# Kernel tuning notes

Hardware: AMD Instinct MI355X
Metric: run time of the kernel (lower is better)

The kernel has to match this reference:

```python
import jax, jax.numpy as jnp
import numpy as np

FEATURE_DIM = 256
NUM_STEPS = 3
NUM_GRAPHS = 2048
ATOMS_PER_GRAPH = 64
TOTAL_ATOMS = NUM_GRAPHS * ATOMS_PER_GRAPH


def setup_inputs() -> dict:
    key = jax.random.key(0)
    k_x, k1, k2, k3, k4 = jax.random.split(key, 5)
    H = FEATURE_DIM
    s = 1.0 / np.sqrt(H)
    x = jax.random.normal(k_x, (TOTAL_ATOMS, H), dtype=jnp.float32)
    batch = jnp.repeat(jnp.arange(NUM_GRAPHS, dtype=jnp.int64), ATOMS_PER_GRAPH)
    sizes = jnp.full((NUM_GRAPHS,), ATOMS_PER_GRAPH, dtype=jnp.int64)
    # LSTM params (PyTorch layout: gates ordered i, f, g, o)
    W_ih = jax.random.uniform(k1, (4 * H, H), jnp.float32, -s, s)
    W_hh = jax.random.uniform(k2, (4 * H, H), jnp.float32, -s, s)
    b_ih = jax.random.uniform(k3, (4 * H,), jnp.float32, -s, s)
    b_hh = jax.random.uniform(k4, (4 * H,), jnp.float32, -s, s)
    return {"x": x, "batch": batch, "sizes": sizes,
            "W_ih": W_ih, "W_hh": W_hh, "b_ih": b_ih, "b_hh": b_hh}


def _lstm_cell(u, hx, cx, W_ih, W_hh, b_ih, b_hh):
    # u: input [B,H]; (hx, cx): hidden/cell [B,H]
    gates = u @ W_ih.T + b_ih + hx @ W_hh.T + b_hh  # [B, 4H]
    i, f, g, o = jnp.split(gates, 4, axis=-1)
    i, f, o = jax.nn.sigmoid(i), jax.nn.sigmoid(f), jax.nn.sigmoid(o)
    c = f * cx + i * jnp.tanh(g)
    h = o * jnp.tanh(c)
    return h, c


def _segment_softmax(scores, seg, num_segments):
    m = jax.ops.segment_max(scores, seg, num_segments=num_segments)
    e = jnp.exp(scores - m[seg])
    s = jax.ops.segment_sum(e, seg, num_segments=num_segments)
    return e / s[seg]


def reference(x, batch, sizes, W_ih, W_hh, b_ih, b_hh):
    B = sizes.shape[0]
    H = x.shape[1]
    seg = batch.astype(jnp.int32)
    h = jnp.zeros((B, H), dtype=x.dtype)
    c = jnp.zeros((B, H), dtype=x.dtype)
    q = h
    r = h
    for _ in range(NUM_STEPS):
        # torch code feeds h both as LSTM input and hidden state
        q, c = _lstm_cell(h, h, c, W_ih, W_hh, b_ih, b_hh)
        scores = jnp.sum(x * q[seg], axis=-1)              # [total_atoms]
        attn = _segment_softmax(scores, seg, B)            # per-graph softmax
        r = jax.ops.segment_sum(x * attn[:, None], seg, num_segments=B)  # [B,H]
        h = r  # torch code overwrites the LSTM hidden with r
    return jnp.concatenate([q, r], axis=-1)  # [B, 2H]
```

## Files before the change

kernel.cpp:

```cpp
#include <hip/hip_runtime.h>
#include <math.h>

#define H 256
#define NB 2048
#define APG 64

typedef __attribute__((ext_vector_type(8))) short short8;
typedef __attribute__((ext_vector_type(4))) float f32x4;

__device__ __forceinline__ unsigned short f2bf(float f) {
    unsigned u = __float_as_uint(f);
    u += 0x7fff + ((u >> 16) & 1);
    return (unsigned short)(u >> 16);
}
__device__ __forceinline__ float bf2f(unsigned short s) {
    return __uint_as_float((unsigned)s << 16);
}
__device__ __forceinline__ float sigm(float v) { return 1.f / (1.f + __expf(-v)); }

__global__ void prep_kernel(const float* __restrict__ W_ih, const float* __restrict__ W_hh,
                            const float* __restrict__ b_ih, const float* __restrict__ b_hh,
                            unsigned short* __restrict__ Wr, float* __restrict__ br) {
    int idx = blockIdx.x * 256 + threadIdx.x;
    int wr_row = idx >> 8, k = idx & 255;
    int hcol = wr_row >> 2, gate = wr_row & 3;
    int src = gate * 65536 + hcol * 256 + k;
    Wr[idx] = f2bf(W_ih[src] + W_hh[src]);
    if (idx < 1024) {
        int hc = idx >> 2, gt = idx & 3;
        br[idx] = b_ih[gt * 256 + hc] + b_hh[gt * 256 + hc];
    }
}

__global__ void lstm0(const float* __restrict__ br, float* __restrict__ q1,
                      float* __restrict__ c1) {
    int hc = threadIdx.x;
    float gi = br[hc * 4 + 0], gg = br[hc * 4 + 2], go = br[hc * 4 + 3];
    float si = sigm(gi), so = sigm(go);
    float cn = si * tanhf(gg);
    c1[hc] = cn;
    q1[hc] = so * tanhf(cn);
}

__global__ __launch_bounds__(256)
void gemm_lstm(const unsigned short* __restrict__ hbf, const unsigned short* __restrict__ Wr,
               const float* __restrict__ br, float* __restrict__ c,
               float* __restrict__ qdst, int qstride) {
    __shared__ unsigned short smem[2][64 * 128];
    unsigned short* As = smem[0];
    unsigned short* Bs = smem[1];
    int t = threadIdx.x;
    int r0 = blockIdx.y * 64;
    int w0 = blockIdx.x * 64;
    int c0h = blockIdx.x * 16;
    int lane = t & 63, w = t >> 6;
    int ln = lane & 15, qd = lane >> 4;
    int m0 = w * 16;
    f32x4 acc[4] = {};
    for (int kc = 0; kc < 2; ++kc) {
        #pragma unroll
        for (int p = 0; p < 4; ++p) {
            int gid = p * 256 + t;
            int row = gid >> 4, g = gid & 15;
            int sg = g ^ (row & 15);
            *(short8*)&As[row * 128 + sg * 8] =
                *(const short8*)&hbf[(r0 + row) * H + kc * 128 + g * 8];
            *(short8*)&Bs[row * 128 + sg * 8] =
                *(const short8*)&Wr[(w0 + row) * H + kc * 128 + g * 8];
        }
        __syncthreads();
        #pragma unroll
        for (int kk = 0; kk < 4; ++kk) {
            int ga = (kk * 4 + qd) ^ ln;
            short8 a = *(short8*)&As[(m0 + ln) * 128 + ga * 8];
            #pragma unroll
            for (int t4 = 0; t4 < 4; ++t4) {
                short8 b = *(short8*)&Bs[(t4 * 16 + ln) * 128 + ga * 8];
                acc[t4] = __builtin_amdgcn_mfma_f32_16x16x32_bf16(a, b, acc[t4], 0, 0, 0);
            }
        }
        __syncthreads();
    }
    float* gl = (float*)smem;
    #pragma unroll
    for (int t4 = 0; t4 < 4; ++t4)
        #pragma unroll
        for (int r = 0; r < 4; ++r)
            gl[(m0 + qd * 4 + r) * 68 + t4 * 16 + ln] = acc[t4][r];
    __syncthreads();
    #pragma unroll
    for (int p = 0; p < 4; ++p) {
        int idx = p * 256 + t;
        int row = idx >> 4, hc = idx & 15;
        float4 g4 = *(float4*)&gl[row * 68 + hc * 4];
        float4 b4 = *(const float4*)&br[(c0h + hc) * 4];
        float gi = g4.x + b4.x, gf = g4.y + b4.y, gg = g4.z + b4.z, go = g4.w + b4.w;
        float si = sigm(gi), sf = sigm(gf), so = sigm(go);
        int cidx = (r0 + row) * H + c0h + hc;
        float cn = sf * c[cidx] + si * tanhf(gg);
        c[cidx] = cn;
        qdst[(r0 + row) * qstride + c0h + hc] = so * tanhf(cn);
    }
}

__global__ __launch_bounds__(256)
void attention1(const float* __restrict__ x, const float* __restrict__ q1,
                unsigned short* __restrict__ hbf, const float* __restrict__ c1,
                float* __restrict__ cdst, unsigned short* __restrict__ xbf) {
    __shared__ float sc[64];
    __shared__ float pl[64];
    __shared__ float rpart[4][256];
    int g = blockIdx.x, t = threadIdx.x;
    int lane = t & 63, w = t >> 6;
    const float* xg = x + (size_t)g * APG * H;
    unsigned short* xbg = xbf + (size_t)g * APG * H;
    float4 xa[16];
    #pragma unroll
    for (int i = 0; i < 16; ++i)
        xa[i] = *(const float4*)&xg[(i * 4 + w) * H + lane * 4];
    float4 q4 = *(const float4*)&q1[lane * 4];
    cdst[g * H + t] = c1[t];
    #pragma unroll
    for (int i = 0; i < 16; ++i) {
        ushort4 u;
        u.x = f2bf(xa[i].x); u.y = f2bf(xa[i].y);
        u.z = f2bf(xa[i].z); u.w = f2bf(xa[i].w);
        *(ushort4*)&xbg[(i * 4 + w) * H + lane * 4] = u;
    }
    #pragma unroll
    for (int i = 0; i < 16; ++i) {
        float p = xa[i].x * q4.x + xa[i].y * q4.y + xa[i].z * q4.z + xa[i].w * q4.w;
        #pragma unroll
        for (int s = 32; s > 0; s >>= 1) p += __shfl_xor(p, s, 64);
        if (lane == 0) sc[i * 4 + w] = p;
    }
    __syncthreads();
    if (t < 64) {
        float s = sc[t], m = s;
        #pragma unroll
        for (int d = 32; d > 0; d >>= 1) m = fmaxf(m, __shfl_xor(m, d, 64));
        float e = __expf(s - m), sum = e;
        #pragma unroll
        for (int d = 32; d > 0; d >>= 1) sum += __shfl_xor(sum, d, 64);
        pl[t] = e / sum;
    }
    __syncthreads();
    float4 r4 = {0.f, 0.f, 0.f, 0.f};
    #pragma unroll
    for (int i = 0; i < 16; ++i) {
        float p = pl[i * 4 + w];
        r4.x += p * xa[i].x; r4.y += p * xa[i].y;
        r4.z += p * xa[i].z; r4.w += p * xa[i].w;
    }
    *(float4*)&rpart[w][lane * 4] = r4;
    __syncthreads();
    float o = rpart[0][t] + rpart[1][t] + rpart[2][t] + rpart[3][t];
    hbf[g * H + t] = f2bf(o);
}

__global__ __launch_bounds__(256)
void attention_bf(const unsigned short* __restrict__ xbf, const float* __restrict__ qsrc,
                  int qstride, unsigned short* __restrict__ hbf,
                  float* __restrict__ rf32, int rstride) {
    __shared__ float sc[64];
    __shared__ float pl[64];
    __shared__ float rpart[4][256];
    int g = blockIdx.x, t = threadIdx.x;
    int lane = t & 63, w = t >> 6;
    const unsigned short* xg = xbf + (size_t)g * APG * H;
    ushort4 xa[16];
    #pragma unroll
    for (int i = 0; i < 16; ++i)
        xa[i] = *(const ushort4*)&xg[(i * 4 + w) * H + lane * 4];
    float4 q4 = *(const float4*)&qsrc[g * qstride + lane * 4];
    #pragma unroll
    for (int i = 0; i < 16; ++i) {
        float p = bf2f(xa[i].x) * q4.x + bf2f(xa[i].y) * q4.y
                + bf2f(xa[i].z) * q4.z + bf2f(xa[i].w) * q4.w;
        #pragma unroll
        for (int s = 32; s > 0; s >>= 1) p += __shfl_xor(p, s, 64);
        if (lane == 0) sc[i * 4 + w] = p;
    }
    __syncthreads();
    if (t < 64) {
        float s = sc[t], m = s;
        #pragma unroll
        for (int d = 32; d > 0; d >>= 1) m = fmaxf(m, __shfl_xor(m, d, 64));
        float e = __expf(s - m), sum = e;
        #pragma unroll
        for (int d = 32; d > 0; d >>= 1) sum += __shfl_xor(sum, d, 64);
        pl[t] = e / sum;
    }
    __syncthreads();
    float4 r4 = {0.f, 0.f, 0.f, 0.f};
    #pragma unroll
    for (int i = 0; i < 16; ++i) {
        float p = pl[i * 4 + w];
        r4.x += p * bf2f(xa[i].x); r4.y += p * bf2f(xa[i].y);
        r4.z += p * bf2f(xa[i].z); r4.w += p * bf2f(xa[i].w);
    }
    *(float4*)&rpart[w][lane * 4] = r4;
    __syncthreads();
    float o = rpart[0][t] + rpart[1][t] + rpart[2][t] + rpart[3][t];
    if (hbf)  hbf[g * H + t] = f2bf(o);
    if (rf32) rf32[g * rstride + t] = o;
}

extern "C" void kernel_launch(void* const* d_in, const int* in_sizes, int n_in,
                              void* d_out, int out_size, void* d_ws, size_t ws_size,
                              hipStream_t stream) {
    const float* x    = (const float*)d_in[0];
    const float* W_ih = (const float*)d_in[3];
    const float* W_hh = (const float*)d_in[4];
    const float* b_ih = (const float*)d_in[5];
    const float* b_hh = (const float*)d_in[6];
    float* out = (float*)d_out;

    char* ws = (char*)d_ws;
    unsigned short* Wr   = (unsigned short*)ws;
    float*          br   = (float*)(ws + 524288);
    unsigned short* hbf  = (unsigned short*)(ws + 528384);
    float*          cbuf = (float*)(ws + 1576960);
    float*          qbuf = (float*)(ws + 3674112);
    float*          q1   = (float*)(ws + 5771264);
    float*          c1   = (float*)(ws + 5772288);
    unsigned short* xbf  = (unsigned short*)(ws + 8388608);

    prep_kernel<<<1024, 256, 0, stream>>>(W_ih, W_hh, b_ih, b_hh, Wr, br);
    lstm0<<<1, 256, 0, stream>>>(br, q1, c1);
    attention1<<<2048, 256, 0, stream>>>(x, q1, hbf, c1, cbuf, xbf);
    gemm_lstm<<<dim3(16, 32), 256, 0, stream>>>(hbf, Wr, br, cbuf, qbuf, 256);
    attention_bf<<<2048, 256, 0, stream>>>(xbf, qbuf, 256, hbf, nullptr, 0);
    gemm_lstm<<<dim3(16, 32), 256, 0, stream>>>(hbf, Wr, br, cbuf, out, 512);
    attention_bf<<<2048, 256, 0, stream>>>(xbf, out, 512, nullptr, out + 256, 512);
}
```

Before: 267.1 us.

## Stream fp32 x in every attention pass instead of caching a bf16 copy

Drops the global bf16 copy of x, which was written once and read twice. Each attention pass now reads fp32 x directly, stages a bf16 copy in shared memory for the weighted sum, and computes scores in fp32. Initial cell-state broadcast moves into a separate 2048-block lstm0b kernel. This removes the 64MB bf16 write but raises each later pass's x read from 64MB to 128MB, and the 32KB shared-memory tile may reduce occupancy.

```diff
diff --git a/kernel.cpp b/kernel.cpp
--- a/kernel.cpp
+++ b/kernel.cpp
@@ -32,14 +32,14 @@
     }
 }
 
-__global__ void lstm0(const float* __restrict__ br, float* __restrict__ q1,
-                      float* __restrict__ c1) {
-    int hc = threadIdx.x;
-    float gi = br[hc * 4 + 0], gg = br[hc * 4 + 2], go = br[hc * 4 + 3];
-    float si = sigm(gi), so = sigm(go);
-    float cn = si * tanhf(gg);
-    c1[hc] = cn;
-    q1[hc] = so * tanhf(cn);
+__global__ __launch_bounds__(256)
+void lstm0b(const float* __restrict__ br, float* __restrict__ q1,
+            float* __restrict__ cbuf) {
+    int g = blockIdx.x, t = threadIdx.x;
+    float4 b4 = *(const float4*)&br[t * 4];
+    float cn1 = sigm(b4.x) * tanhf(b4.z);
+    cbuf[(size_t)g * H + t] = cn1;
+    if (g == 0) q1[t] = sigm(b4.w) * tanhf(cn1);
 }
 
 __global__ __launch_bounds__(256)
@@ -104,37 +104,32 @@
 }
 
 __global__ __launch_bounds__(256)
-void attention1(const float* __restrict__ x, const float* __restrict__ q1,
-                unsigned short* __restrict__ hbf, const float* __restrict__ c1,
-                float* __restrict__ cdst, unsigned short* __restrict__ xbf) {
+void attn(const float* __restrict__ x, const float* __restrict__ qsrc, int qstride,
+          unsigned short* __restrict__ hbf_out, float* __restrict__ rout, int rstride) {
+    __shared__ __align__(16) unsigned short xl[APG * H];
     __shared__ float sc[64];
     __shared__ float pl[64];
-    __shared__ float rpart[4][256];
+    __shared__ __align__(16) float rpart[4][256];
     int g = blockIdx.x, t = threadIdx.x;
     int lane = t & 63, w = t >> 6;
     const float* xg = x + (size_t)g * APG * H;
-    unsigned short* xbg = xbf + (size_t)g * APG * H;
-    float4 xa[16];
-    #pragma unroll
-    for (int i = 0; i < 16; ++i)
-        xa[i] = *(const float4*)&xg[(i * 4 + w) * H + lane * 4];
-    float4 q4 = *(const float4*)&q1[lane * 4];
-    cdst[g * H + t] = c1[t];
+
+    float4 q4 = *(const float4*)&qsrc[(size_t)g * qstride + lane * 4];
+
     #pragma unroll
     for (int i = 0; i < 16; ++i) {
+        int row = i * 4 + w;
+        float4 f = *(const float4*)&xg[row * H + lane * 4];
         ushort4 u;
-        u.x = f2bf(xa[i].x); u.y = f2bf(xa[i].y);
-        u.z = f2bf(xa[i].z); u.w = f2bf(xa[i].w);
-        *(ushort4*)&xbg[(i * 4 + w) * H + lane * 4] = u;
-    }
-    #pragma unroll
-    for (int i = 0; i < 16; ++i) {
-        float p = xa[i].x * q4.x + xa[i].y * q4.y + xa[i].z * q4.z + xa[i].w * q4.w;
+        u.x = f2bf(f.x); u.y = f2bf(f.y); u.z = f2bf(f.z); u.w = f2bf(f.w);
+        *(ushort4*)&xl[row * H + lane * 4] = u;
+        float p = f.x * q4.x + f.y * q4.y + f.z * q4.z + f.w * q4.w;
         #pragma unroll
-        for (int s = 32; s > 0; s >>= 1) p += __shfl_xor(p, s, 64);
-        if (lane == 0) sc[i * 4 + w] = p;
+        for (int d = 32; d > 0; d >>= 1) p += __shfl_xor(p, d, 64);
+        if (lane == 0) sc[row] = p;
     }
     __syncthreads();
+
     if (t < 64) {
         float s = sc[t], m = s;
         #pragma unroll
@@ -145,65 +140,21 @@
         pl[t] = e / sum;
     }
     __syncthreads();
+
     float4 r4 = {0.f, 0.f, 0.f, 0.f};
     #pragma unroll
     for (int i = 0; i < 16; ++i) {
-        float p = pl[i * 4 + w];
-        r4.x += p * xa[i].x; r4.y += p * xa[i].y;
-        r4.z += p * xa[i].z; r4.w += p * xa[i].w;
+        int row = i * 4 + w;
+        float p = pl[row];
+        ushort4 u = *(ushort4*)&xl[row * H + lane * 4];
+        r4.x += p * bf2f(u.x); r4.y += p * bf2f(u.y);
+        r4.z += p * bf2f(u.z); r4.w += p * bf2f(u.w);
     }
     *(float4*)&rpart[w][lane * 4] = r4;
     __syncthreads();
     float o = rpart[0][t] + rpart[1][t] + rpart[2][t] + rpart[3][t];
-    hbf[g * H + t] = f2bf(o);
-}
-
-__global__ __launch_bounds__(256)
-void attention_bf(const unsigned short* __restrict__ xbf, const float* __restrict__ qsrc,
-                  int qstride, unsigned short* __restrict__ hbf,
-                  float* __restrict__ rf32, int rstride) {
-    __shared__ float sc[64];
-    __shared__ float pl[64];
-    __shared__ float rpart[4][256];
-    int g = blockIdx.x, t = threadIdx.x;
-    int lane = t & 63, w = t >> 6;
-    const unsigned short* xg = xbf + (size_t)g * APG * H;
-    ushort4 xa[16];
-    #pragma unroll
-    for (int i = 0; i < 16; ++i)
-        xa[i] = *(const ushort4*)&xg[(i * 4 + w) * H + lane * 4];
-    float4 q4 = *(const float4*)&qsrc[g * qstride + lane * 4];
-    #pragma unroll
-    for (int i = 0; i < 16; ++i) {
-        float p = bf2f(xa[i].x) * q4.x + bf2f(xa[i].y) * q4.y
-                + bf2f(xa[i].z) * q4.z + bf2f(xa[i].w) * q4.w;
-        #pragma unroll
-        for (int s = 32; s > 0; s >>= 1) p += __shfl_xor(p, s, 64);
-        if (lane == 0) sc[i * 4 + w] = p;
-    }
-    __syncthreads();
-    if (t < 64) {
-        float s = sc[t], m = s;
-        #pragma unroll
-        for (int d = 32; d > 0; d >>= 1) m = fmaxf(m, __shfl_xor(m, d, 64));
-        float e = __expf(s - m), sum = e;
-        #pragma unroll
-        for (int d = 32; d > 0; d >>= 1) sum += __shfl_xor(sum, d, 64);
-        pl[t] = e / sum;
-    }
-    __syncthreads();
-    float4 r4 = {0.f, 0.f, 0.f, 0.f};
-    #pragma unroll
-    for (int i = 0; i < 16; ++i) {
-        float p = pl[i * 4 + w];
-        r4.x += p * bf2f(xa[i].x); r4.y += p * bf2f(xa[i].y);
-        r4.z += p * bf2f(xa[i].z); r4.w += p * bf2f(xa[i].w);
-    }
-    *(float4*)&rpart[w][lane * 4] = r4;
-    __syncthreads();
-    float o = rpart[0][t] + rpart[1][t] + rpart[2][t] + rpart[3][t];
-    if (hbf)  hbf[g * H + t] = f2bf(o);
-    if (rf32) rf32[g * rstride + t] = o;
+    if (hbf_out) hbf_out[(size_t)g * H + t] = f2bf(o);
+    if (rout)    rout[(size_t)g * rstride + t] = o;
 }
 
 extern "C" void kernel_launch(void* const* d_in, const int* in_sizes, int n_in,
@@ -219,18 +170,16 @@
     char* ws = (char*)d_ws;
     unsigned short* Wr   = (unsigned short*)ws;
     float*          br   = (float*)(ws + 524288);
-    unsigned short* hbf  = (unsigned short*)(ws + 528384);
-    float*          cbuf = (float*)(ws + 1576960);
-    float*          qbuf = (float*)(ws + 3674112);
-    float*          q1   = (float*)(ws + 5771264);
-    float*          c1   = (float*)(ws + 5772288);
-    unsigned short* xbf  = (unsigned short*)(ws + 8388608);
+    float*          q1   = (float*)(ws + 528384);
+    float*          cbuf = (float*)(ws + 532480);
+    float*          qbuf = (float*)(ws + 2629632);
+    unsigned short* hbf  = (unsigned short*)(ws + 4726784);
 
     prep_kernel<<<1024, 256, 0, stream>>>(W_ih, W_hh, b_ih, b_hh, Wr, br);
-    lstm0<<<1, 256, 0, stream>>>(br, q1, c1);
-    attention1<<<2048, 256, 0, stream>>>(x, q1, hbf, c1, cbuf, xbf);
+    lstm0b<<<2048, 256, 0, stream>>>(br, q1, cbuf);
+    attn<<<2048, 256, 0, stream>>>(x, q1, 0, hbf, nullptr, 0);
     gemm_lstm<<<dim3(16, 32), 256, 0, stream>>>(hbf, Wr, br, cbuf, qbuf, 256);
-    attention_bf<<<2048, 256, 0, stream>>>(xbf, qbuf, 256, hbf, nullptr, 0);
+    attn<<<2048, 256, 0, stream>>>(x, qbuf, 256, hbf, nullptr, 0);
     gemm_lstm<<<dim3(16, 32), 256, 0, stream>>>(hbf, Wr, br, cbuf, out, 512);
-    attention_bf<<<2048, 256, 0, stream>>>(xbf, out, 512, nullptr, out + 256, 512);
+    attn<<<2048, 256, 0, stream>>>(x, out, 512, nullptr, out + 256, 512);
 }
```

After: 267.8 us. Within noise of the previous version (+0.3%).
